# Performance work log

Measured on AMD Instinct MI355X. Metric: run time of the kernel, lower is better.

Reference implementation:

```python
import jax, jax.numpy as jnp
import numpy as np

N = 50000      # nodes
E = 800000     # edges (avg in-degree 16)
IN_DIM = 128
OUT_DIM = 64
LEAKY_SLOPE = 0.01  # torch F.leaky_relu default


def setup_inputs() -> dict:
    key = jax.random.key(0)
    ks = jax.random.split(key, 7)
    h = jax.random.normal(ks[0], (N, IN_DIM), dtype=jnp.float32)
    r_h = jax.random.normal(ks[1], (E, OUT_DIM), dtype=jnp.float32)
    edge_src = jax.random.randint(ks[2], (E,), 0, N, dtype=jnp.int32)
    edge_dst = jax.random.randint(ks[3], (E,), 0, N, dtype=jnp.int32)
    # learned params (xavier-ish scaling)
    W_fc = jax.random.normal(ks[4], (OUT_DIM, IN_DIM), dtype=jnp.float32) * (1.0 / np.sqrt(IN_DIM))
    attn_w = jax.random.normal(ks[5], (1, 3 * OUT_DIM), dtype=jnp.float32) * 0.1
    loop_weight = jax.random.normal(ks[6], (OUT_DIM, OUT_DIM), dtype=jnp.float32) * (1.0 / np.sqrt(OUT_DIM))
    return {"h": h, "r_h": r_h, "W_fc": W_fc, "attn_w": attn_w,
            "loop_weight": loop_weight, "edge_src": edge_src, "edge_dst": edge_dst}


def reference(h, r_h, W_fc, attn_w, loop_weight, edge_src, edge_dst):
    # z = fc(h)   [N, OUT_DIM]
    z = h @ W_fc.T
    z_src = z[edge_src]          # [E, OUT_DIM]
    z_dst = z[edge_dst]          # [E, OUT_DIM]
    # attn_fc(cat([z_src, z_dst, r_h])) expressed without materializing the concat
    w1 = attn_w[0, :OUT_DIM]
    w2 = attn_w[0, OUT_DIM:2 * OUT_DIM]
    w3 = attn_w[0, 2 * OUT_DIM:]
    a = z_src @ w1 + z_dst @ w2 + r_h @ w3            # [E]
    e = jax.nn.leaky_relu(a, LEAKY_SLOPE)
    # segment softmax over incoming edges of each destination node
    seg_max = jax.ops.segment_max(e, edge_dst, num_segments=N)  # -inf for deg-0 (never gathered)
    e_exp = jnp.exp(e - jax.lax.stop_gradient(seg_max)[edge_dst])
    denom = jax.ops.segment_sum(e_exp, edge_dst, num_segments=N)
    alpha = e_exp / denom[edge_dst]                   # [E]
    # weighted scatter-sum of source features
    agg = jax.ops.segment_sum(alpha[:, None] * z_src, edge_dst, num_segments=N)  # [N, OUT_DIM]
    # DGL only runs reduce_func (incl. self-loop matmul) on nodes with in-edges
    deg = jax.ops.segment_sum(jnp.ones((E,), jnp.float32), edge_dst, num_segments=N)
    h_out = jnp.where(deg[:, None] > 0, agg + z @ loop_weight, 0.0)
    return jax.nn.relu(h_out)
```

## Files before the change

### kernel.cpp

```cpp
#include <hip/hip_runtime.h>

#define NN 50000
#define EE 800000
#define IND 128
#define OUTD 64
#define NB 49

__global__ __launch_bounds__(256) void k_pass_a(
    const float* __restrict__ h, const float* __restrict__ W,
    const float* __restrict__ attn, float* __restrict__ z,
    float* __restrict__ s1, float* __restrict__ s2) {
  __shared__ float Wl[64 * 129];
  const int tid = threadIdx.x;
#pragma unroll
  for (int j = 0; j < 8; ++j) {
    int i4 = tid + j * 256;
    const float4 v = reinterpret_cast<const float4*>(W)[i4];
    int i = i4 * 4;
    int col = i >> 7, k = i & 127;
    float* p = &Wl[col * 129 + k];
    p[0] = v.x; p[1] = v.y; p[2] = v.z; p[3] = v.w;
  }
  __syncthreads();
  const int lane = tid & 63;
  const int wid = tid >> 6;
  float Wreg[128];
#pragma unroll
  for (int k = 0; k < 128; ++k) Wreg[k] = Wl[lane * 129 + k];
  const float w1v = attn[lane];
  const float w2v = attn[64 + lane];
  const int base = blockIdx.x * 64 + wid * 16;
  for (int i = 0; i < 16; ++i) {
    int r = base + i;
    if (r >= NN) return;
    const float* hr = h + (size_t)r * IND;
    float h0 = hr[lane];
    float h1 = hr[64 + lane];
    float acc = 0.f;
#pragma unroll
    for (int k = 0; k < 64; ++k)
      acc = fmaf(__uint_as_float(__builtin_amdgcn_readlane(__float_as_uint(h0), k)),
                 Wreg[k], acc);
#pragma unroll
    for (int k = 0; k < 64; ++k)
      acc = fmaf(__uint_as_float(__builtin_amdgcn_readlane(__float_as_uint(h1), k)),
                 Wreg[64 + k], acc);
    z[(size_t)r * OUTD + lane] = acc;
    float p = acc * w1v, q = acc * w2v;
#pragma unroll
    for (int m = 32; m >= 1; m >>= 1) {
      p += __shfl_xor(p, m, 64);
      q += __shfl_xor(q, m, 64);
    }
    if (lane == 0) { s1[r] = p; s2[r] = q; }
  }
}

__global__ __launch_bounds__(256) void k_pass_b(
    const float* __restrict__ r_h, const float* __restrict__ attn,
    const int* __restrict__ esrc, const int* __restrict__ edst,
    const float* __restrict__ s1, const float* __restrict__ s2,
    float* __restrict__ ee, int* __restrict__ deg) {
  const int t = blockIdx.x * 256 + threadIdx.x;
  const int sub = t & 15;
  float4 rv = reinterpret_cast<const float4*>(r_h)[t];
  float4 wv = reinterpret_cast<const float4*>(attn + 2 * OUTD)[sub];
  float d = rv.x * wv.x + rv.y * wv.y + rv.z * wv.z + rv.w * wv.w;
  d += __shfl_xor(d, 1, 64);
  d += __shfl_xor(d, 2, 64);
  d += __shfl_xor(d, 4, 64);
  d += __shfl_xor(d, 8, 64);
  if (sub == 0) {
    const int e = t >> 4;
    int s = esrc[e], dd = edst[e];
    float a = s1[s] + s2[dd] + d;
    float el = a > 0.f ? a : 0.01f * a;
    ee[e] = __expf(el);
    atomicAdd(&deg[dd], 1);
  }
}

__global__ __launch_bounds__(1024) void k_scan1(
    const int* __restrict__ deg, int* __restrict__ offL,
    int* __restrict__ blocksum) {
  __shared__ int wsum[16];
  __shared__ int woff[17];
  const int tid = threadIdx.x;
  const int gid = blockIdx.x * 1024 + tid;
  const int lane = tid & 63, wid = tid >> 6;
  int v = (gid < NN) ? deg[gid] : 0;
  int incl = v;
#pragma unroll
  for (int o = 1; o < 64; o <<= 1) {
    int t = __shfl_up(incl, o, 64);
    if (lane >= o) incl += t;
  }
  if (lane == 63) wsum[wid] = incl;
  __syncthreads();
  if (wid == 0 && lane < 16) {
    int s = wsum[lane];
    int si = s;
#pragma unroll
    for (int o = 1; o < 16; o <<= 1) {
      int t = __shfl_up(si, o, 64);
      if (lane >= o) si += t;
    }
    woff[lane] = si - s;
    if (lane == 15) woff[16] = si;
  }
  __syncthreads();
  if (gid < NN) offL[gid] = woff[wid] + incl - v;
  if (tid == 0) blocksum[blockIdx.x] = woff[16];
}

__global__ __launch_bounds__(64) void k_scan2(
    const int* __restrict__ blocksum, int* __restrict__ blockoff) {
  const int lane = threadIdx.x;
  int v = (lane < NB) ? blocksum[lane] : 0;
  int incl = v;
#pragma unroll
  for (int o = 1; o < 64; o <<= 1) {
    int t = __shfl_up(incl, o, 64);
    if (lane >= o) incl += t;
  }
  if (lane < NB) blockoff[lane] = incl - v;
}

__global__ __launch_bounds__(256) void k_scatter(
    const int* __restrict__ esrc, const int* __restrict__ edst,
    const float* __restrict__ ee, const int* __restrict__ offL,
    const int* __restrict__ blockoff, int* __restrict__ cursor,
    int2* __restrict__ pairs) {
  const int e = blockIdx.x * 256 + threadIdx.x;
  if (e >= EE) return;
  int d = edst[e];
  int pos = blockoff[d >> 10] + offL[d] + atomicAdd(&cursor[d], 1);
  pairs[pos] = make_int2(esrc[e], __float_as_int(ee[e]));
}

__global__ __launch_bounds__(256) void k_agg(
    const float* __restrict__ z, const int2* __restrict__ pairs,
    const int* __restrict__ offL, const int* __restrict__ blockoff,
    const int* __restrict__ deg, const float* __restrict__ LW,
    float* __restrict__ out) {
  const int lane = threadIdx.x & 63, wid = threadIdx.x >> 6;
  float LWreg[64];
#pragma unroll
  for (int k = 0; k < 64; ++k) LWreg[k] = LW[k * OUTD + lane];
  const int r = blockIdx.x * 4 + wid;
  if (r >= NN) return;
  const int cnt = deg[r];
  const int2* pp = pairs + (blockoff[r >> 10] + offL[r]);
  float acc = 0.f, wsum = 0.f;
  int i = 0;
  for (; i + 4 <= cnt; i += 4) {
    int2 p0 = pp[i], p1 = pp[i + 1], p2 = pp[i + 2], p3 = pp[i + 3];
    float a0 = z[(size_t)p0.x * OUTD + lane];
    float a1 = z[(size_t)p1.x * OUTD + lane];
    float a2 = z[(size_t)p2.x * OUTD + lane];
    float a3 = z[(size_t)p3.x * OUTD + lane];
    float w0 = __int_as_float(p0.y), w1 = __int_as_float(p1.y);
    float w2 = __int_as_float(p2.y), w3 = __int_as_float(p3.y);
    acc = fmaf(w0, a0, acc);
    acc = fmaf(w1, a1, acc);
    acc = fmaf(w2, a2, acc);
    acc = fmaf(w3, a3, acc);
    wsum += (w0 + w1) + (w2 + w3);
  }
  for (; i < cnt; ++i) {
    int2 p = pp[i];
    float w = __int_as_float(p.y);
    acc = fmaf(w, z[(size_t)p.x * OUTD + lane], acc);
    wsum += w;
  }
  float zv = z[(size_t)r * OUTD + lane];
  float lacc = 0.f;
#pragma unroll
  for (int k = 0; k < 64; ++k)
    lacc = fmaf(__uint_as_float(__builtin_amdgcn_readlane(__float_as_uint(zv), k)),
                LWreg[k], lacc);
  float res = 0.f;
  if (cnt > 0) {
    float v = acc / wsum + lacc;
    res = v > 0.f ? v : 0.f;
  }
  out[(size_t)r * OUTD + lane] = res;
}

extern "C" void kernel_launch(void* const* d_in, const int* in_sizes, int n_in,
                              void* d_out, int out_size, void* d_ws, size_t ws_size,
                              hipStream_t stream) {
  const float* h    = (const float*)d_in[0];
  const float* r_h  = (const float*)d_in[1];
  const float* W_fc = (const float*)d_in[2];
  const float* attn = (const float*)d_in[3];
  const float* LW   = (const float*)d_in[4];
  const int* esrc   = (const int*)d_in[5];
  const int* edst   = (const int*)d_in[6];
  float* out = (float*)d_out;

  char* ws = (char*)d_ws;
  float* z      = (float*)(ws);
  float* ee     = (float*)(ws + 12800000);
  int2*  pairs  = (int2*)(ws + 16000000);
  float* s1     = (float*)(ws + 22400000);
  float* s2     = (float*)(ws + 22600000);
  int*   deg    = (int*)(ws + 22800000);
  int*   cursor = (int*)(ws + 23000000);
  int*   offL   = (int*)(ws + 23200000);
  int*   bsum   = (int*)(ws + 23400000);
  int*   boff   = (int*)(ws + 23401024);

  hipMemsetAsync(deg, 0, (size_t)NN * sizeof(int), stream);
  hipMemsetAsync(cursor, 0, (size_t)NN * sizeof(int), stream);

  k_pass_a<<<(NN + 63) / 64, 256, 0, stream>>>(h, W_fc, attn, z, s1, s2);
  k_pass_b<<<EE * 16 / 256, 256, 0, stream>>>(r_h, attn, esrc, edst, s1, s2, ee, deg);
  k_scan1<<<NB, 1024, 0, stream>>>(deg, offL, bsum);
  k_scan2<<<1, 64, 0, stream>>>(bsum, boff);
  k_scatter<<<(EE + 255) / 256, 256, 0, stream>>>(esrc, edst, ee, offL, boff, cursor, pairs);
  k_agg<<<(NN + 3) / 4, 256, 0, stream>>>(z, pairs, offL, boff, deg, LW, out);
}
```

Measured before the change: 473.6 us.

## Precompute edge ranks in degree pass, fuse attention with CSR scatter, vectorize aggregation

Degree counting moves to its own kernel, which records each edge's slot within its destination node. This lets the attention-score kernel write (src, exp) pairs straight into CSR order, removing the ee buffer, the cursor memset and the separate scatter kernel with its atomics. The aggregation kernel now has each wave process four edges in parallel using float4 z loads, then reduces the partial sums with cross-lane shuffles. The self-loop matvec is also restructured to use float4 weights. The cost is an extra edge-wide pass plus the rank buffer, and the bounds check on the row index is dropped, which relies on NN being divisible by 4.

```diff
diff --git a/kernel.cpp b/kernel.cpp
--- a/kernel.cpp
+++ b/kernel.cpp
@@ -5,6 +5,12 @@
 #define IND 128
 #define OUTD 64
 #define NB 49
+
+__global__ __launch_bounds__(256) void k_deg(
+    const int* __restrict__ edst, int* __restrict__ deg, int* __restrict__ rank) {
+  const int e = blockIdx.x * 256 + threadIdx.x;
+  if (e < EE) rank[e] = atomicAdd(&deg[edst[e]], 1);
+}
 
 __global__ __launch_bounds__(256) void k_pass_a(
     const float* __restrict__ h, const float* __restrict__ W,
@@ -56,11 +62,58 @@
   }
 }
 
-__global__ __launch_bounds__(256) void k_pass_b(
+__global__ __launch_bounds__(1024) void k_scan1(
+    const int* __restrict__ deg, int* __restrict__ offL,
+    int* __restrict__ blocksum) {
+  __shared__ int wsum[16];
+  __shared__ int woff[17];
+  const int tid = threadIdx.x;
+  const int gid = blockIdx.x * 1024 + tid;
+  const int lane = tid & 63, wid = tid >> 6;
+  int v = (gid < NN) ? deg[gid] : 0;
+  int incl = v;
+#pragma unroll
+  for (int o = 1; o < 64; o <<= 1) {
+    int t = __shfl_up(incl, o, 64);
+    if (lane >= o) incl += t;
+  }
+  if (lane == 63) wsum[wid] = incl;
+  __syncthreads();
+  if (wid == 0 && lane < 16) {
+    int s = wsum[lane];
+    int si = s;
+#pragma unroll
+    for (int o = 1; o < 16; o <<= 1) {
+      int t = __shfl_up(si, o, 64);
+      if (lane >= o) si += t;
+    }
+    woff[lane] = si - s;
+    if (lane == 15) woff[16] = si;
+  }
+  __syncthreads();
+  if (gid < NN) offL[gid] = woff[wid] + incl - v;
+  if (tid == 0) blocksum[blockIdx.x] = woff[16];
+}
+
+__global__ __launch_bounds__(64) void k_scan2(
+    const int* __restrict__ blocksum, int* __restrict__ blockoff) {
+  const int lane = threadIdx.x;
+  int v = (lane < NB) ? blocksum[lane] : 0;
+  int incl = v;
+#pragma unroll
+  for (int o = 1; o < 64; o <<= 1) {
+    int t = __shfl_up(incl, o, 64);
+    if (lane >= o) incl += t;
+  }
+  if (lane < NB) blockoff[lane] = incl - v;
+}
+
+__global__ __launch_bounds__(256) void k_attn_scatter(
     const float* __restrict__ r_h, const float* __restrict__ attn,
     const int* __restrict__ esrc, const int* __restrict__ edst,
     const float* __restrict__ s1, const float* __restrict__ s2,
-    float* __restrict__ ee, int* __restrict__ deg) {
+    const int* __restrict__ rank, const int* __restrict__ offL,
+    const int* __restrict__ blockoff, int2* __restrict__ pairs) {
   const int t = blockIdx.x * 256 + threadIdx.x;
   const int sub = t & 15;
   float4 rv = reinterpret_cast<const float4*>(r_h)[t];
@@ -75,67 +128,10 @@
     int s = esrc[e], dd = edst[e];
     float a = s1[s] + s2[dd] + d;
     float el = a > 0.f ? a : 0.01f * a;
-    ee[e] = __expf(el);
-    atomicAdd(&deg[dd], 1);
-  }
-}
-
-__global__ __launch_bounds__(1024) void k_scan1(
-    const int* __restrict__ deg, int* __restrict__ offL,
-    int* __restrict__ blocksum) {
-  __shared__ int wsum[16];
-  __shared__ int woff[17];
-  const int tid = threadIdx.x;
-  const int gid = blockIdx.x * 1024 + tid;
-  const int lane = tid & 63, wid = tid >> 6;
-  int v = (gid < NN) ? deg[gid] : 0;
-  int incl = v;
-#pragma unroll
-  for (int o = 1; o < 64; o <<= 1) {
-    int t = __shfl_up(incl, o, 64);
-    if (lane >= o) incl += t;
-  }
-  if (lane == 63) wsum[wid] = incl;
-  __syncthreads();
-  if (wid == 0 && lane < 16) {
-    int s = wsum[lane];
-    int si = s;
-#pragma unroll
-    for (int o = 1; o < 16; o <<= 1) {
-      int t = __shfl_up(si, o, 64);
-      if (lane >= o) si += t;
-    }
-    woff[lane] = si - s;
-    if (lane == 15) woff[16] = si;
-  }
-  __syncthreads();
-  if (gid < NN) offL[gid] = woff[wid] + incl - v;
-  if (tid == 0) blocksum[blockIdx.x] = woff[16];
-}
-
-__global__ __launch_bounds__(64) void k_scan2(
-    const int* __restrict__ blocksum, int* __restrict__ blockoff) {
-  const int lane = threadIdx.x;
-  int v = (lane < NB) ? blocksum[lane] : 0;
-  int incl = v;
-#pragma unroll
-  for (int o = 1; o < 64; o <<= 1) {
-    int t = __shfl_up(incl, o, 64);
-    if (lane >= o) incl += t;
-  }
-  if (lane < NB) blockoff[lane] = incl - v;
-}
-
-__global__ __launch_bounds__(256) void k_scatter(
-    const int* __restrict__ esrc, const int* __restrict__ edst,
-    const float* __restrict__ ee, const int* __restrict__ offL,
-    const int* __restrict__ blockoff, int* __restrict__ cursor,
-    int2* __restrict__ pairs) {
-  const int e = blockIdx.x * 256 + threadIdx.x;
-  if (e >= EE) return;
-  int d = edst[e];
-  int pos = blockoff[d >> 10] + offL[d] + atomicAdd(&cursor[d], 1);
-  pairs[pos] = make_int2(esrc[e], __float_as_int(ee[e]));
+    float ex = __expf(el);
+    int pos = blockoff[dd >> 10] + offL[dd] + rank[e];
+    pairs[pos] = make_int2(s, __float_as_int(ex));
+  }
 }
 
 __global__ __launch_bounds__(256) void k_agg(
@@ -144,47 +140,69 @@
     const int* __restrict__ deg, const float* __restrict__ LW,
     float* __restrict__ out) {
   const int lane = threadIdx.x & 63, wid = threadIdx.x >> 6;
-  float LWreg[64];
-#pragma unroll
-  for (int k = 0; k < 64; ++k) LWreg[k] = LW[k * OUTD + lane];
+  const int slot = lane >> 4, sub = lane & 15;
+  float4 LWreg[16];
+#pragma unroll
+  for (int kl = 0; kl < 16; ++kl)
+    LWreg[kl] = reinterpret_cast<const float4*>(LW)[(slot * 16 + kl) * 16 + sub];
   const int r = blockIdx.x * 4 + wid;
-  if (r >= NN) return;
   const int cnt = deg[r];
   const int2* pp = pairs + (blockoff[r >> 10] + offL[r]);
-  float acc = 0.f, wsum = 0.f;
-  int i = 0;
-  for (; i + 4 <= cnt; i += 4) {
-    int2 p0 = pp[i], p1 = pp[i + 1], p2 = pp[i + 2], p3 = pp[i + 3];
-    float a0 = z[(size_t)p0.x * OUTD + lane];
-    float a1 = z[(size_t)p1.x * OUTD + lane];
-    float a2 = z[(size_t)p2.x * OUTD + lane];
-    float a3 = z[(size_t)p3.x * OUTD + lane];
-    float w0 = __int_as_float(p0.y), w1 = __int_as_float(p1.y);
-    float w2 = __int_as_float(p2.y), w3 = __int_as_float(p3.y);
-    acc = fmaf(w0, a0, acc);
-    acc = fmaf(w1, a1, acc);
-    acc = fmaf(w2, a2, acc);
-    acc = fmaf(w3, a3, acc);
-    wsum += (w0 + w1) + (w2 + w3);
-  }
-  for (; i < cnt; ++i) {
-    int2 p = pp[i];
-    float w = __int_as_float(p.y);
-    acc = fmaf(w, z[(size_t)p.x * OUTD + lane], acc);
-    wsum += w;
-  }
-  float zv = z[(size_t)r * OUTD + lane];
-  float lacc = 0.f;
-#pragma unroll
-  for (int k = 0; k < 64; ++k)
-    lacc = fmaf(__uint_as_float(__builtin_amdgcn_readlane(__float_as_uint(zv), k)),
-                LWreg[k], lacc);
-  float res = 0.f;
-  if (cnt > 0) {
-    float v = acc / wsum + lacc;
-    res = v > 0.f ? v : 0.f;
-  }
-  out[(size_t)r * OUTD + lane] = res;
+  float4 acc = make_float4(0.f, 0.f, 0.f, 0.f);
+  float wsum = 0.f;
+  for (int i = 0; i < cnt; i += 8) {
+    int e0 = i + slot, e1 = i + 4 + slot;
+    bool v0 = e0 < cnt, v1 = e1 < cnt;
+    int2 p0 = pp[v0 ? e0 : 0];
+    int2 p1 = pp[v1 ? e1 : 0];
+    float4 z0 = reinterpret_cast<const float4*>(z)[(size_t)p0.x * 16 + sub];
+    float4 z1 = reinterpret_cast<const float4*>(z)[(size_t)p1.x * 16 + sub];
+    float w0 = v0 ? __int_as_float(p0.y) : 0.f;
+    float w1 = v1 ? __int_as_float(p1.y) : 0.f;
+    acc.x = fmaf(w0, z0.x, acc.x);
+    acc.y = fmaf(w0, z0.y, acc.y);
+    acc.z = fmaf(w0, z0.z, acc.z);
+    acc.w = fmaf(w0, z0.w, acc.w);
+    acc.x = fmaf(w1, z1.x, acc.x);
+    acc.y = fmaf(w1, z1.y, acc.y);
+    acc.z = fmaf(w1, z1.z, acc.z);
+    acc.w = fmaf(w1, z1.w, acc.w);
+    wsum += w0 + w1;
+  }
+  float4 lacc = make_float4(0.f, 0.f, 0.f, 0.f);
+#pragma unroll
+  for (int j = 0; j < 4; ++j) {
+    float4 zq = reinterpret_cast<const float4*>(z)[(size_t)r * 16 + slot * 4 + j];
+    float zk[4] = {zq.x, zq.y, zq.z, zq.w};
+#pragma unroll
+    for (int c = 0; c < 4; ++c) {
+      float4 lw = LWreg[4 * j + c];
+      lacc.x = fmaf(zk[c], lw.x, lacc.x);
+      lacc.y = fmaf(zk[c], lw.y, lacc.y);
+      lacc.z = fmaf(zk[c], lw.z, lacc.z);
+      lacc.w = fmaf(zk[c], lw.w, lacc.w);
+    }
+  }
+  wsum += __shfl_xor(wsum, 16, 64);
+  wsum += __shfl_xor(wsum, 32, 64);
+  float inv = (cnt > 0) ? 1.f / wsum : 0.f;
+  float4 t;
+  t.x = fmaf(acc.x, inv, lacc.x);
+  t.y = fmaf(acc.y, inv, lacc.y);
+  t.z = fmaf(acc.z, inv, lacc.z);
+  t.w = fmaf(acc.w, inv, lacc.w);
+  t.x += __shfl_xor(t.x, 16, 64); t.x += __shfl_xor(t.x, 32, 64);
+  t.y += __shfl_xor(t.y, 16, 64); t.y += __shfl_xor(t.y, 32, 64);
+  t.z += __shfl_xor(t.z, 16, 64); t.z += __shfl_xor(t.z, 32, 64);
+  t.w += __shfl_xor(t.w, 16, 64); t.w += __shfl_xor(t.w, 32, 64);
+  if (slot == 0) {
+    float4 res;
+    res.x = (cnt > 0 && t.x > 0.f) ? t.x : 0.f;
+    res.y = (cnt > 0 && t.y > 0.f) ? t.y : 0.f;
+    res.z = (cnt > 0 && t.z > 0.f) ? t.z : 0.f;
+    res.w = (cnt > 0 && t.w > 0.f) ? t.w : 0.f;
+    reinterpret_cast<float4*>(out)[(size_t)r * 16 + sub] = res;
+  }
 }
 
 extern "C" void kernel_launch(void* const* d_in, const int* in_sizes, int n_in,
@@ -200,24 +218,23 @@
   float* out = (float*)d_out;
 
   char* ws = (char*)d_ws;
-  float* z      = (float*)(ws);
-  float* ee     = (float*)(ws + 12800000);
-  int2*  pairs  = (int2*)(ws + 16000000);
-  float* s1     = (float*)(ws + 22400000);
-  float* s2     = (float*)(ws + 22600000);
-  int*   deg    = (int*)(ws + 22800000);
-  int*   cursor = (int*)(ws + 23000000);
-  int*   offL   = (int*)(ws + 23200000);
-  int*   bsum   = (int*)(ws + 23400000);
-  int*   boff   = (int*)(ws + 23401024);
+  float* z     = (float*)(ws);
+  int2*  pairs = (int2*)(ws + 12800000);
+  int*   rank  = (int*)(ws + 19200000);
+  float* s1    = (float*)(ws + 22400000);
+  float* s2    = (float*)(ws + 22600000);
+  int*   deg   = (int*)(ws + 22800000);
+  int*   offL  = (int*)(ws + 23000000);
+  int*   bsum  = (int*)(ws + 23200000);
+  int*   boff  = (int*)(ws + 23201024);
 
   hipMemsetAsync(deg, 0, (size_t)NN * sizeof(int), stream);
-  hipMemsetAsync(cursor, 0, (size_t)NN * sizeof(int), stream);
-
+
+  k_deg<<<(EE + 255) / 256, 256, 0, stream>>>(edst, deg, rank);
   k_pass_a<<<(NN + 63) / 64, 256, 0, stream>>>(h, W_fc, attn, z, s1, s2);
-  k_pass_b<<<EE * 16 / 256, 256, 0, stream>>>(r_h, attn, esrc, edst, s1, s2, ee, deg);
   k_scan1<<<NB, 1024, 0, stream>>>(deg, offL, bsum);
   k_scan2<<<1, 64, 0, stream>>>(bsum, boff);
-  k_scatter<<<(EE + 255) / 256, 256, 0, stream>>>(esrc, edst, ee, offL, boff, cursor, pairs);
-  k_agg<<<(NN + 3) / 4, 256, 0, stream>>>(z, pairs, offL, boff, deg, LW, out);
-}
+  k_attn_scatter<<<EE * 16 / 256, 256, 0, stream>>>(
+      r_h, attn, esrc, edst, s1, s2, rank, offL, boff, pairs);
+  k_agg<<<NN / 4, 256, 0, stream>>>(z, pairs, offL, boff, deg, LW, out);
+}
```

After: 461.0 us. 1.03x faster.
